# Optimization experiments

Measured on AMD Instinct MI355X. Metric: run time of the kernel, lower is better.

Reference implementation:

```python
import jax, jax.numpy as jnp
import numpy as np

B, T, E, H, V = 32, 128, 512, 1024, 32000


def setup_inputs() -> dict:
    key = jax.random.key(0)
    ks = jax.random.split(key, 14)
    s = 0.02  # param init scale to keep gates in a sane range
    return {
        "features": jax.random.normal(ks[0], (B, E), jnp.float32),
        "captions": jax.random.randint(ks[1], (B, T), 0, V, jnp.int64),
        "embed_table": jax.random.normal(ks[2], (V, E), jnp.float32) * s,
        "pos_enc": jax.random.normal(ks[3], (1, T, E), jnp.float32) * s,
        "W_ih0": jax.random.normal(ks[4], (4 * H, E), jnp.float32) * s,
        "W_hh0": jax.random.normal(ks[5], (4 * H, H), jnp.float32) * s,
        "b_ih0": jax.random.normal(ks[6], (4 * H,), jnp.float32) * s,
        "b_hh0": jax.random.normal(ks[7], (4 * H,), jnp.float32) * s,
        "W_ih1": jax.random.normal(ks[8], (4 * H, H), jnp.float32) * s,
        "W_hh1": jax.random.normal(ks[9], (4 * H, H), jnp.float32) * s,
        "b_ih1": jax.random.normal(ks[10], (4 * H,), jnp.float32) * s,
        "b_hh1": jax.random.normal(ks[11], (4 * H,), jnp.float32) * s,
        "W_out": jax.random.normal(ks[12], (V, H), jnp.float32) * s,
        "b_out": jax.random.normal(ks[13], (V,), jnp.float32) * s,
    }


def _lstm_cell(h, c, x, W_ih, W_hh, b_ih, b_hh):
    # PyTorch gate order: i, f, g, o
    g = x @ W_ih.T + b_ih + h @ W_hh.T + b_hh  # (B, 4H)
    i, f, gg, o = jnp.split(g, 4, axis=-1)
    c_new = jax.nn.sigmoid(f) * c + jax.nn.sigmoid(i) * jnp.tanh(gg)
    h_new = jax.nn.sigmoid(o) * jnp.tanh(c_new)
    return h_new, c_new


def reference(features, captions, embed_table, pos_enc,
              W_ih0, W_hh0, b_ih0, b_hh0,
              W_ih1, W_hh1, b_ih1, b_hh1,
              W_out, b_out):
    # Teacher forcing ratio = 1.0 (the default): the input at step t is
    # captions[:, t-1], so the whole sequence of inputs is known upfront.
    bsz, seqlen = captions.shape
    hdim = W_hh0.shape[1]
    vocab = W_out.shape[0]
    dt = embed_table.dtype

    # Embedding lookup for all steps; only pos_enc[:, :1, :] is ever added.
    x = embed_table[captions[:, : seqlen - 1]] + pos_enc[0, 0]  # (B, T-1, E)
    x = jnp.swapaxes(x, 0, 1)  # (T-1, B, E) time-major for scan

    h0 = jnp.zeros((bsz, hdim), dt)
    c0 = jnp.zeros((bsz, hdim), dt)
    h1 = jnp.zeros((bsz, hdim), dt)
    c1 = jnp.zeros((bsz, hdim), dt)

    def step(carry, x_t):
        h0, c0, h1, c1 = carry
        h0, c0 = _lstm_cell(h0, c0, x_t, W_ih0, W_hh0, b_ih0, b_hh0)
        h1, c1 = _lstm_cell(h1, c1, h0, W_ih1, W_hh1, b_ih1, b_hh1)
        return (h0, c0, h1, c1), h1

    _, hs = jax.lax.scan(step, (h0, c0, h1, c1), x)  # (T-1, B, H)

    # One big GEMM for the decode projection of all steps.
    logits = jnp.einsum('tbh,vh->btv', hs, W_out) + b_out  # (B, T-1, V)
    outputs = jnp.concatenate(
        [jnp.zeros((bsz, 1, vocab), dt), logits], axis=1)  # outputs[:,0,:]=0
    return outputs
```

## Files before the change

### kernel.cpp

```cpp
#include <hip/hip_runtime.h>
#include <hip/hip_bf16.h>
#include <math.h>

typedef __attribute__((ext_vector_type(4))) float f32x4;
typedef __attribute__((ext_vector_type(8))) short s16x8;
typedef __attribute__((ext_vector_type(4))) unsigned short u16x4;

#define MFMA16(a, b, c) __builtin_amdgcn_mfma_f32_16x16x32_bf16(a, b, c, 0, 0, 0)

static constexpr int BB = 32, TT = 128, EE = 512, HH = 1024, VV = 32000;
static constexpr int FH = 4 * HH;
static constexpr int MROWS = (TT - 1) * BB;
static constexpr int MPAD = 4096;
static constexpr int BH = BB * HH;
static constexpr int NBLK = 256;

__device__ __forceinline__ unsigned short f2bf(float f) {
  unsigned int u = __float_as_uint(f);
  u = (u + 0x7FFFu + ((u >> 16) & 1u)) >> 16;
  return (unsigned short)u;
}
__device__ __forceinline__ float sigf(float x) { return 1.f / (1.f + __expf(-x)); }

__device__ __forceinline__ s16x8 pack8f(const float* p) {
  float4 x = *(const float4*)p;
  float4 y = *(const float4*)(p + 4);
  s16x8 r;
  r[0] = (short)f2bf(x.x); r[1] = (short)f2bf(x.y);
  r[2] = (short)f2bf(x.z); r[3] = (short)f2bf(x.w);
  r[4] = (short)f2bf(y.x); r[5] = (short)f2bf(y.y);
  r[6] = (short)f2bf(y.z); r[7] = (short)f2bf(y.w);
  return r;
}

__device__ __forceinline__ void gl_lds16(const void* g, void* l) {
  __builtin_amdgcn_global_load_lds(
      (const __attribute__((address_space(1))) unsigned int*)g,
      (__attribute__((address_space(3))) unsigned int*)l, 16, 0, 0);
}

__device__ __forceinline__ unsigned ldflag(const unsigned int* p) {
  return __hip_atomic_load(p, __ATOMIC_RELAXED, __HIP_MEMORY_SCOPE_AGENT);
}


__global__ void zero2_k(uint4* __restrict__ p0, int n0, uint4* __restrict__ p1, int n1) {
  int i = blockIdx.x * blockDim.x + threadIdx.x;
  int stride = gridDim.x * blockDim.x;
  uint4 z = {0u, 0u, 0u, 0u};
  for (int k = i; k < n0; k += stride) p0[k] = z;
  for (int k = i; k < n1; k += stride) p1[k] = z;
}

__global__ void cvt2_k(const float4* __restrict__ a, u16x4* __restrict__ ao, int na4,
                       const float4* __restrict__ b, u16x4* __restrict__ bo, int nb4) {
  int i = blockIdx.x * blockDim.x + threadIdx.x;
  int stride = gridDim.x * blockDim.x;
  for (int k = i; k < na4; k += stride) {
    float4 v = a[k];
    u16x4 o;
    o[0] = f2bf(v.x); o[1] = f2bf(v.y); o[2] = f2bf(v.z); o[3] = f2bf(v.w);
    ao[k] = o;
  }
  for (int k = i; k < nb4; k += stride) {
    float4 v = b[k];
    u16x4 o;
    o[0] = f2bf(v.x); o[1] = f2bf(v.y); o[2] = f2bf(v.z); o[3] = f2bf(v.w);
    bo[k] = o;
  }
}

__global__ __launch_bounds__(256) void embed_k(const int* __restrict__ captions,
                                               const float* __restrict__ etab,
                                               const float* __restrict__ pos,
                                               unsigned short* __restrict__ X) {
  const int m = blockIdx.x;
  const int t = m >> 5, b = m & 31;
  if (t < TT - 1) {
    const int tok = captions[b * TT + t];
    const float* er = etab + (size_t)tok * EE;
    for (int e = threadIdx.x; e < EE; e += 256)
      X[(size_t)m * EE + e] = f2bf(er[e] + pos[e]);
  } else {
    for (int e = threadIdx.x; e < EE; e += 256) X[(size_t)m * EE + e] = 0;
  }
}

__global__ void zero_out_t0(float* __restrict__ out) {
  out[(size_t)blockIdx.y * TT * VV + blockIdx.x * 256 + threadIdx.x] = 0.f;
}


__global__ __launch_bounds__(256) void gemm_bt(const unsigned short* __restrict__ A,
                                               const unsigned short* __restrict__ Bm,
                                               int K, int N,
                                               const float* __restrict__ bias0,
                                               const float* __restrict__ bias1,
                                               float* __restrict__ Cout) {
  __shared__ unsigned short As[128 * 64];
  __shared__ unsigned short Bs[128 * 64];
  const int tid = threadIdx.x;
  const int lane = tid & 63, wave = tid >> 6;
  const int wm = wave & 1, wn = wave >> 1;
  const int m0 = blockIdx.x * 128, n0 = blockIdx.y * 128;
  const int sch = (((lane & 7) ^ ((lane >> 3) & 7)) * 8);
  const int srbase = wave * 32 + (lane >> 3);
  f32x4 acc[4][4] = {};

  for (int k0 = 0; k0 < K; k0 += 64) {
    __syncthreads();
#pragma unroll
    for (int i = 0; i < 4; ++i) {
      const int r = srbase + i * 8;
      gl_lds16(&A[(size_t)(m0 + r) * K + k0 + sch], &As[(wave * 4 + i) * 512]);
      gl_lds16(&Bm[(size_t)(n0 + r) * K + k0 + sch], &Bs[(wave * 4 + i) * 512]);
    }
    __syncthreads();
#pragma unroll
    for (int kk = 0; kk < 64; kk += 32) {
      s16x8 af[4], bf[4];
#pragma unroll
      for (int f = 0; f < 4; ++f) {
        const int Ra = wm * 64 + f * 16 + (lane & 15);
        const int Rb = wn * 64 + f * 16 + (lane & 15);
        const int slot = (kk >> 3) + (lane >> 4);
        af[f] = *(const s16x8*)(&As[Ra * 64 + ((slot ^ (Ra & 7)) * 8)]);
        bf[f] = *(const s16x8*)(&Bs[Rb * 64 + ((slot ^ (Rb & 7)) * 8)]);
      }
#pragma unroll
      for (int mi = 0; mi < 4; ++mi)
#pragma unroll
        for (int ni = 0; ni < 4; ++ni)
          acc[mi][ni] = MFMA16(af[mi], bf[ni], acc[mi][ni]);
    }
  }

#pragma unroll
  for (int mi = 0; mi < 4; ++mi) {
#pragma unroll
    for (int ni = 0; ni < 4; ++ni) {
      const int col = n0 + wn * 64 + ni * 16 + (lane & 15);
      float bs = bias0[col] + bias1[col];
      const int mbase = m0 + wm * 64 + mi * 16 + (lane >> 4) * 4;
#pragma unroll
      for (int r = 0; r < 4; ++r) {
        int m = mbase + r;
        if (m < MROWS) Cout[(size_t)m * N + col] = acc[mi][ni][r] + bs;
      }
    }
  }
}


__global__ __launch_bounds__(512, 1) void proj_gemm(const unsigned short* __restrict__ hsA,
                                                    const unsigned short* __restrict__ Woutb,
                                                    const float* __restrict__ bout,
                                                    float* __restrict__ out) {
  __shared__ unsigned short As[2][256 * 64];
  __shared__ unsigned short Bs[2][256 * 64];
  const int tid = threadIdx.x;
  const int lane = tid & 63, wave = tid >> 6;
  const int wm = wave & 1, wn = wave >> 1;
  const int T = blockIdx.x;
  const int bq = T & 15;
  const int j = 2 * (bq & 7) + (bq >> 3);
  const int n = T >> 4;
  const int m0 = j * 256, n0 = n * 256;
  const int sch = (((lane & 7) ^ ((lane >> 3) & 7)) * 8);
  const int rbase = tid >> 3;
  f32x4 acc[8][4] = {};

  auto stageP = [&](int ks, int buf) {
    const int k0 = ks * 64;
#pragma unroll
    for (int i = 0; i < 4; ++i) {
      const int r = rbase + i * 64;
      gl_lds16(&hsA[(size_t)(m0 + r) * HH + k0 + sch], &As[buf][(wave * 64 + i * 512) * 8]);
      gl_lds16(&Woutb[(size_t)(n0 + r) * HH + k0 + sch], &Bs[buf][(wave * 64 + i * 512) * 8]);
    }
  };

  stageP(0, 0);

  for (int ks = 0; ks < 16; ++ks) {
    const int cur = ks & 1;
    if (ks < 15) {
      stageP(ks + 1, cur ^ 1);
      asm volatile("s_waitcnt vmcnt(8)" ::: "memory");
    } else {
      asm volatile("s_waitcnt vmcnt(0)" ::: "memory");
    }
    __builtin_amdgcn_s_barrier();
#pragma unroll
    for (int kk = 0; kk < 64; kk += 32) {
      s16x8 af[8], bf[4];
#pragma unroll
      for (int f = 0; f < 8; ++f) {
        const int Ra = wm * 128 + f * 16 + (lane & 15);
        const int slot = (kk >> 3) + (lane >> 4);
        af[f] = *(const s16x8*)(&As[cur][Ra * 64 + ((slot ^ (Ra & 7)) * 8)]);
      }
#pragma unroll
      for (int f = 0; f < 4; ++f) {
        const int Rb = wn * 64 + f * 16 + (lane & 15);
        const int slot = (kk >> 3) + (lane >> 4);
        bf[f] = *(const s16x8*)(&Bs[cur][Rb * 64 + ((slot ^ (Rb & 7)) * 8)]);
      }
#pragma unroll
      for (int mi = 0; mi < 8; ++mi)
#pragma unroll
        for (int ni = 0; ni < 4; ++ni)
          acc[mi][ni] = MFMA16(af[mi], bf[ni], acc[mi][ni]);
    }
    asm volatile("" ::: "memory");
    __builtin_amdgcn_s_barrier();
  }

#pragma unroll
  for (int mi = 0; mi < 8; ++mi) {
#pragma unroll
    for (int ni = 0; ni < 4; ++ni) {
      const int col = n0 + wn * 64 + ni * 16 + (lane & 15);
      const float bs = bout[col];
      const int mbase = m0 + wm * 128 + mi * 16 + (lane >> 4) * 4;
#pragma unroll
      for (int r2 = 0; r2 < 4; ++r2) {
        const int m = mbase + r2;
        if (m < MROWS) {
          const int tt = m >> 5, b2 = m & 31;
          out[((size_t)b2 * TT + tt + 1) * VV + col] = acc[mi][ni][r2] + bs;
        }
      }
    }
  }
}


__global__ __launch_bounds__(256, 1) void lstm_persist(
    const float* __restrict__ Whh0f, const float* __restrict__ Wih1f,
    const float* __restrict__ Whh1f, const float* __restrict__ G0pre,
    const float* __restrict__ bih1, const float* __restrict__ bhh1,
    unsigned short* __restrict__ h0seq, unsigned short* __restrict__ hseq1,
    unsigned short* __restrict__ hs_all,
    unsigned int* __restrict__ flags0, unsigned int* __restrict__ flags1) {
  __shared__ float parts[4][2][2][16][16];
  const int bid = blockIdx.x;
  const int layer = bid >> 7;
  const int blk = bid & 127;
  const int tid = threadIdx.x, lane = tid & 63, wave = tid >> 6;
  const int jb = blk * 8;
  const int colIdx = lane & 15;
  const int kq = lane >> 4;
  const int wrow0 = (colIdx >> 3) * HH + jb + (colIdx & 7);

  const int cb = tid >> 3, cjj = tid & 7;
  float creg = 0.f;
  float bsum[4];
  if (layer == 1) {
#pragma unroll
    for (int gi = 0; gi < 4; ++gi)
      bsum[gi] = bih1[gi * HH + jb + cjj] + bhh1[gi * HH + jb + cjj];
  }

  s16x8 wreg[16][2];
  const int kb = (layer == 0) ? wave * 256 : (wave & 1) * 512;
  if (layer == 0) {
#pragma unroll
    for (int fi = 0; fi < 2; ++fi) {
      const float* wp = Whh0f + (size_t)(wrow0 + fi * 2 * HH) * HH + kb + kq * 8;
#pragma unroll
      for (int ks = 0; ks < 8; ++ks) wreg[ks][fi] = pack8f(wp + ks * 32);
    }
  } else {
    const float* Wsrc = (wave < 2) ? Wih1f : Whh1f;
#pragma unroll
    for (int fi = 0; fi < 2; ++fi) {
      const float* wp = Wsrc + (size_t)(wrow0 + fi * 2 * HH) * HH + kb + kq * 8;
#pragma unroll
      for (int ks = 0; ks < 16; ++ks) wreg[ks][fi] = pack8f(wp + ks * 32);
    }
  }

  const int frag_off = (kb >> 3) * 256 + kq * 256 + (lane & 15) * 8;

  if (layer == 0) {
    for (int t = 0; t < TT - 1; ++t) {
      float gpre[4];
#pragma unroll
      for (int gi = 0; gi < 4; ++gi)
        gpre[gi] = G0pre[((size_t)t * BB + cb) * FH + gi * HH + jb + cjj];

      if (t > 0 && wave == 0) {
        const unsigned tgt = (unsigned)t;
        for (;;) {
          unsigned a = ldflag(&flags0[(lane * 2 + 0) * 32]);
          unsigned b = ldflag(&flags0[(lane * 2 + 1) * 32]);
          if (__all(min(a, b) >= tgt)) break;
          __builtin_amdgcn_s_sleep(1);
        }
      }
      __syncthreads();
      asm volatile("" ::: "memory");

      const unsigned short* a0 = h0seq + (size_t)t * BH + frag_off;
      const unsigned short* a1 = a0 + 128;
      f32x4 acc00 = {}, acc01 = {}, acc10 = {}, acc11 = {};
#pragma unroll
      for (int ks = 0; ks < 8; ++ks) {
        s16x8 av0 = *(const s16x8*)(a0 + ks * 1024);
        s16x8 av1 = *(const s16x8*)(a1 + ks * 1024);
        acc00 = MFMA16(av0, wreg[ks][0], acc00);
        acc01 = MFMA16(av0, wreg[ks][1], acc01);
        acc10 = MFMA16(av1, wreg[ks][0], acc10);
        acc11 = MFMA16(av1, wreg[ks][1], acc11);
      }
#pragma unroll
      for (int r = 0; r < 4; ++r) {
        parts[wave][0][0][kq * 4 + r][colIdx] = acc00[r];
        parts[wave][0][1][kq * 4 + r][colIdx] = acc01[r];
        parts[wave][1][0][kq * 4 + r][colIdx] = acc10[r];
        parts[wave][1][1][kq * 4 + r][colIdx] = acc11[r];
      }
      __syncthreads();
      float g[4];
#pragma unroll
      for (int gi = 0; gi < 4; ++gi) {
        float s = gpre[gi];
        const int fi = gi >> 1, c = (gi & 1) * 8 + cjj;
#pragma unroll
        for (int w4 = 0; w4 < 4; ++w4) s += parts[w4][cb >> 4][fi][cb & 15][c];
        g[gi] = s;
      }
      const float i_ = sigf(g[0]), f_ = sigf(g[1]), gg = tanhf(g[2]), o_ = sigf(g[3]);
      creg = f_ * creg + i_ * gg;
      *(volatile unsigned short*)&h0seq[(size_t)(t + 1) * BH + blk * 256 + tid] =
          f2bf(o_ * tanhf(creg));

      asm volatile("s_waitcnt vmcnt(0)" ::: "memory");
      __syncthreads();
      if (tid == 0) *(volatile unsigned int*)&flags0[blk * 32] = (unsigned)(t + 1);
    }
  } else {
    for (int t = 1; t < TT; ++t) {
      if (wave == 0) {
        const unsigned t0 = (unsigned)t, t1 = (unsigned)(t - 1);
        for (;;) {
          unsigned a0 = ldflag(&flags0[(lane * 2 + 0) * 32]);
          unsigned b0 = ldflag(&flags0[(lane * 2 + 1) * 32]);
          unsigned a1 = ldflag(&flags1[(lane * 2 + 0) * 32]);
          unsigned b1 = ldflag(&flags1[(lane * 2 + 1) * 32]);
          bool ok = (min(a0, b0) >= t0) && (min(a1, b1) >= t1);
          if (__all(ok)) break;
          __builtin_amdgcn_s_sleep(1);
        }
      }
      __syncthreads();
      asm volatile("" ::: "memory");

      const unsigned short* base = (wave < 2)
                                       ? (h0seq + (size_t)t * BH)
                                       : (hseq1 + (size_t)(t - 1) * BH);
      const unsigned short* a0 = base + frag_off;
      const unsigned short* a1 = a0 + 128;
      f32x4 acc00 = {}, acc01 = {}, acc10 = {}, acc11 = {};
#pragma unroll
      for (int ks = 0; ks < 16; ++ks) {
        s16x8 av0 = *(const s16x8*)(a0 + ks * 1024);
        s16x8 av1 = *(const s16x8*)(a1 + ks * 1024);
        acc00 = MFMA16(av0, wreg[ks][0], acc00);
        acc01 = MFMA16(av0, wreg[ks][1], acc01);
        acc10 = MFMA16(av1, wreg[ks][0], acc10);
        acc11 = MFMA16(av1, wreg[ks][1], acc11);
      }
#pragma unroll
      for (int r = 0; r < 4; ++r) {
        parts[wave][0][0][kq * 4 + r][colIdx] = acc00[r];
        parts[wave][0][1][kq * 4 + r][colIdx] = acc01[r];
        parts[wave][1][0][kq * 4 + r][colIdx] = acc10[r];
        parts[wave][1][1][kq * 4 + r][colIdx] = acc11[r];
      }
      __syncthreads();
      float g[4];
#pragma unroll
      for (int gi = 0; gi < 4; ++gi) {
        float s = bsum[gi];
        const int fi = gi >> 1, c = (gi & 1) * 8 + cjj;
#pragma unroll
        for (int w4 = 0; w4 < 4; ++w4) s += parts[w4][cb >> 4][fi][cb & 15][c];
        g[gi] = s;
      }
      const float i_ = sigf(g[0]), f_ = sigf(g[1]), gg = tanhf(g[2]), o_ = sigf(g[3]);
      creg = f_ * creg + i_ * gg;
      const unsigned short hv = f2bf(o_ * tanhf(creg));
      *(volatile unsigned short*)&hseq1[(size_t)t * BH + blk * 256 + tid] = hv;
      hs_all[(size_t)t * BH + (size_t)cb * HH + jb + cjj] = hv;

      asm volatile("s_waitcnt vmcnt(0)" ::: "memory");
      __syncthreads();
      if (tid == 0) *(volatile unsigned int*)&flags1[blk * 32] = (unsigned)t;
    }
  }
}


extern "C" void kernel_launch(void* const* d_in, const int* in_sizes, int n_in,
                              void* d_out, int out_size, void* d_ws, size_t ws_size,
                              hipStream_t stream) {
  const int* captions = (const int*)d_in[1];
  const float* etab = (const float*)d_in[2];
  const float* pos = (const float*)d_in[3];
  const float* Wih0 = (const float*)d_in[4];
  const float* Whh0 = (const float*)d_in[5];
  const float* bih0 = (const float*)d_in[6];
  const float* bhh0 = (const float*)d_in[7];
  const float* Wih1 = (const float*)d_in[8];
  const float* Whh1 = (const float*)d_in[9];
  const float* bih1 = (const float*)d_in[10];
  const float* bhh1 = (const float*)d_in[11];
  const float* Wout = (const float*)d_in[12];
  const float* bout = (const float*)d_in[13];
  float* out = (float*)d_out;

  char* w = (char*)d_ws;
  auto alloc = [&](size_t bytes) {
    char* p = w;
    w += (bytes + 255) & ~(size_t)255;
    return p;
  };
  unsigned int* flags0 = (unsigned int*)alloc(128 * 128);
  unsigned int* flags1 = (unsigned int*)alloc(128 * 128);
  unsigned short* h0seq = (unsigned short*)alloc((size_t)TT * BH * 2);
  unsigned short* hseq1 = (unsigned short*)alloc((size_t)TT * BH * 2);
  unsigned short* hs_all = (unsigned short*)alloc((size_t)4160 * HH * 2);

  unsigned short* Xb = (unsigned short*)alloc((size_t)MPAD * EE * 2);
  unsigned short* Wih0b = (unsigned short*)alloc((size_t)FH * EE * 2);
  unsigned short* Woutb = (unsigned short*)alloc((size_t)VV * HH * 2);
  float* G0pre = (float*)alloc((size_t)MROWS * FH * 4);

  hipLaunchKernelGGL(zero2_k, dim3(40), dim3(256), 0, stream,
                     (uint4*)flags0, (int)((128 * 128 * 2 + BH * 2) / 16),
                     (uint4*)hseq1, (int)((BH * 2) / 16));
  hipLaunchKernelGGL(cvt2_k, dim3(4096), dim3(256), 0, stream,
                     (const float4*)Wih0, (u16x4*)Wih0b, FH * EE / 4,
                     (const float4*)Wout, (u16x4*)Woutb, VV * HH / 4);
  hipLaunchKernelGGL(embed_k, dim3(MPAD), dim3(256), 0, stream, captions, etab, pos, Xb);
  hipLaunchKernelGGL(gemm_bt, dim3(32, 32), dim3(256), 0, stream, Xb, Wih0b, EE, FH, bih0,
                     bhh0, G0pre);
  hipLaunchKernelGGL(lstm_persist, dim3(NBLK), dim3(256), 0, stream, Whh0, Wih1, Whh1, G0pre,
                     bih1, bhh1, h0seq, hseq1, hs_all, flags0, flags1);
  hipLaunchKernelGGL(proj_gemm, dim3(2000), dim3(512), 0, stream, hs_all + (size_t)BH,
                     Woutb, bout, out);
  hipLaunchKernelGGL(zero_out_t0, dim3(125, 32), dim3(256), 0, stream, out);
}
```

Baseline: 1.265 ms.

## Tune LSTM flag polling, fuse t0 zeroing into projection GEMM, add MFMA priority

Shrinks the flag stride from 32 to 16 words and changes the spin-wait to check once, then sleep longer before polling with a coarser sleep. This is meant to cut polling traffic on the recurrent critical path. Separately, the t=0 output zeroing moves into the projection GEMM, which removes one kernel launch. s_setprio is raised around the MFMA loop. The longer sleeps risk adding wake-up latency on every timestep of the serial recurrence.

```diff
diff --git a/kernel.cpp b/kernel.cpp
--- a/kernel.cpp
+++ b/kernel.cpp
@@ -42,6 +42,8 @@
 __device__ __forceinline__ unsigned ldflag(const unsigned int* p) {
   return __hip_atomic_load(p, __ATOMIC_RELAXED, __HIP_MEMORY_SCOPE_AGENT);
 }
+
+#define FSTRIDE 16
 
 
 __global__ void zero2_k(uint4* __restrict__ p0, int n0, uint4* __restrict__ p1, int n1) {
@@ -84,10 +86,6 @@
   } else {
     for (int e = threadIdx.x; e < EE; e += 256) X[(size_t)m * EE + e] = 0;
   }
-}
-
-__global__ void zero_out_t0(float* __restrict__ out) {
-  out[(size_t)blockIdx.y * TT * VV + blockIdx.x * 256 + threadIdx.x] = 0.f;
 }
 
 
@@ -191,6 +189,7 @@
       asm volatile("s_waitcnt vmcnt(0)" ::: "memory");
     }
     __builtin_amdgcn_s_barrier();
+    __builtin_amdgcn_s_setprio(1);
 #pragma unroll
     for (int kk = 0; kk < 64; kk += 32) {
       s16x8 af[8], bf[4];
@@ -212,6 +211,7 @@
         for (int ni = 0; ni < 4; ++ni)
           acc[mi][ni] = MFMA16(af[mi], bf[ni], acc[mi][ni]);
     }
+    __builtin_amdgcn_s_setprio(0);
     asm volatile("" ::: "memory");
     __builtin_amdgcn_s_barrier();
   }
@@ -231,6 +231,13 @@
           out[((size_t)b2 * TT + tt + 1) * VV + col] = acc[mi][ni][r2] + bs;
         }
       }
+    }
+  }
+
+  if (j == 0) {
+    for (int i = tid; i < 32 * 256; i += 512) {
+      const int b2 = i >> 8, c = i & 255;
+      out[(size_t)b2 * TT * VV + n0 + c] = 0.f;
     }
   }
 }
@@ -292,11 +299,16 @@
 
       if (t > 0 && wave == 0) {
         const unsigned tgt = (unsigned)t;
-        for (;;) {
-          unsigned a = ldflag(&flags0[(lane * 2 + 0) * 32]);
-          unsigned b = ldflag(&flags0[(lane * 2 + 1) * 32]);
-          if (__all(min(a, b) >= tgt)) break;
-          __builtin_amdgcn_s_sleep(1);
+        unsigned a = ldflag(&flags0[(lane * 2 + 0) * FSTRIDE]);
+        unsigned b = ldflag(&flags0[(lane * 2 + 1) * FSTRIDE]);
+        if (!__all(min(a, b) >= tgt)) {
+          __builtin_amdgcn_s_sleep(20);
+          for (;;) {
+            a = ldflag(&flags0[(lane * 2 + 0) * FSTRIDE]);
+            b = ldflag(&flags0[(lane * 2 + 1) * FSTRIDE]);
+            if (__all(min(a, b) >= tgt)) break;
+            __builtin_amdgcn_s_sleep(5);
+          }
         }
       }
       __syncthreads();
@@ -338,20 +350,28 @@
 
       asm volatile("s_waitcnt vmcnt(0)" ::: "memory");
       __syncthreads();
-      if (tid == 0) *(volatile unsigned int*)&flags0[blk * 32] = (unsigned)(t + 1);
+      if (tid == 0) *(volatile unsigned int*)&flags0[blk * FSTRIDE] = (unsigned)(t + 1);
     }
   } else {
     for (int t = 1; t < TT; ++t) {
       if (wave == 0) {
         const unsigned t0 = (unsigned)t, t1 = (unsigned)(t - 1);
-        for (;;) {
-          unsigned a0 = ldflag(&flags0[(lane * 2 + 0) * 32]);
-          unsigned b0 = ldflag(&flags0[(lane * 2 + 1) * 32]);
-          unsigned a1 = ldflag(&flags1[(lane * 2 + 0) * 32]);
-          unsigned b1 = ldflag(&flags1[(lane * 2 + 1) * 32]);
-          bool ok = (min(a0, b0) >= t0) && (min(a1, b1) >= t1);
-          if (__all(ok)) break;
-          __builtin_amdgcn_s_sleep(1);
+        unsigned a0 = ldflag(&flags0[(lane * 2 + 0) * FSTRIDE]);
+        unsigned b0 = ldflag(&flags0[(lane * 2 + 1) * FSTRIDE]);
+        unsigned a1 = ldflag(&flags1[(lane * 2 + 0) * FSTRIDE]);
+        unsigned b1 = ldflag(&flags1[(lane * 2 + 1) * FSTRIDE]);
+        bool ok = (min(a0, b0) >= t0) && (min(a1, b1) >= t1);
+        if (!__all(ok)) {
+          __builtin_amdgcn_s_sleep(20);
+          for (;;) {
+            a0 = ldflag(&flags0[(lane * 2 + 0) * FSTRIDE]);
+            b0 = ldflag(&flags0[(lane * 2 + 1) * FSTRIDE]);
+            a1 = ldflag(&flags1[(lane * 2 + 0) * FSTRIDE]);
+            b1 = ldflag(&flags1[(lane * 2 + 1) * FSTRIDE]);
+            ok = (min(a0, b0) >= t0) && (min(a1, b1) >= t1);
+            if (__all(ok)) break;
+            __builtin_amdgcn_s_sleep(5);
+          }
         }
       }
       __syncthreads();
@@ -397,7 +417,7 @@
 
       asm volatile("s_waitcnt vmcnt(0)" ::: "memory");
       __syncthreads();
-      if (tid == 0) *(volatile unsigned int*)&flags1[blk * 32] = (unsigned)t;
+      if (tid == 0) *(volatile unsigned int*)&flags1[blk * FSTRIDE] = (unsigned)t;
     }
   }
 }
@@ -427,8 +447,8 @@
     w += (bytes + 255) & ~(size_t)255;
     return p;
   };
-  unsigned int* flags0 = (unsigned int*)alloc(128 * 128);
-  unsigned int* flags1 = (unsigned int*)alloc(128 * 128);
+  unsigned int* flags0 = (unsigned int*)alloc(128 * 64);
+  unsigned int* flags1 = (unsigned int*)alloc(128 * 64);
   unsigned short* h0seq = (unsigned short*)alloc((size_t)TT * BH * 2);
   unsigned short* hseq1 = (unsigned short*)alloc((size_t)TT * BH * 2);
   unsigned short* hs_all = (unsigned short*)alloc((size_t)4160 * HH * 2);
@@ -439,7 +459,7 @@
   float* G0pre = (float*)alloc((size_t)MROWS * FH * 4);
 
   hipLaunchKernelGGL(zero2_k, dim3(40), dim3(256), 0, stream,
-                     (uint4*)flags0, (int)((128 * 128 * 2 + BH * 2) / 16),
+                     (uint4*)flags0, (int)((128 * 64 * 2 + BH * 2) / 16),
                      (uint4*)hseq1, (int)((BH * 2) / 16));
   hipLaunchKernelGGL(cvt2_k, dim3(4096), dim3(256), 0, stream,
                      (const float4*)Wih0, (u16x4*)Wih0b, FH * EE / 4,
@@ -451,5 +471,4 @@
                      bih1, bhh1, h0seq, hseq1, hs_all, flags0, flags1);
   hipLaunchKernelGGL(proj_gemm, dim3(2000), dim3(512), 0, stream, hs_all + (size_t)BH,
                      Woutb, bout, out);
-  hipLaunchKernelGGL(zero_out_t0, dim3(125, 32), dim3(256), 0, stream, out);
-}
+}
```

Result: no change. 1.285 ms (+1.6%).
